# Optimization experiments

Measured on AMD Instinct MI355X. Metric: run time of the kernel, lower is better.

Reference implementation:

```python
import jax, jax.numpy as jnp
import numpy as np

H = 2048   # hidden_size
I = 4096   # intermediate_size (expert_dim_per_shard, world_size=1)
E = 8      # num_local_experts


def setup_inputs() -> dict:
    key = jax.random.key(0)
    ks = jax.random.split(key, 7)
    s = 0.02
    return {
        "hidden_states": jax.random.normal(ks[0], (1, 2048, H), dtype=jnp.float32),
        "router_w": jax.random.normal(ks[1], (H, E), dtype=jnp.float32) * s,
        "gate_up_proj": jax.random.normal(ks[2], (E, H, 2 * I), dtype=jnp.float32) * s,
        "down_proj": jax.random.normal(ks[3], (E, I, H), dtype=jnp.float32) * s,
        "shared_gate_w": jax.random.normal(ks[4], (H, I), dtype=jnp.float32) * s,
        "shared_up_w": jax.random.normal(ks[5], (H, I), dtype=jnp.float32) * s,
        "shared_down_w": jax.random.normal(ks[6], (I, H), dtype=jnp.float32) * s,
        "top_k": 1,
    }


def reference(hidden_states, router_w, gate_up_proj, down_proj,
              shared_gate_w, shared_up_w, shared_down_w, top_k):
    b, s, h = hidden_states.shape
    hs = hidden_states.reshape(-1, h)                      # [T, H]
    T = hs.shape[0]

    # router + topk scatter (non-topk -> -inf so sigmoid -> 0)
    logits = hs @ router_w                                 # [T, E]
    top_v, top_i = jax.lax.top_k(logits, top_k)            # [T, k]
    neg_inf = jnp.full_like(logits, -jnp.inf)
    rows = jnp.arange(T)[:, None]
    router_scores = neg_inf.at[rows, top_i].set(top_v).T   # [E, T]
    router_scores = jax.nn.sigmoid(router_scores.astype(jnp.float32)).astype(hs.dtype)

    # dense dispatch: every token to every expert, scaled by (mostly zero) scores
    routed_in = hs[None, :, :] * router_scores[:, :, None]  # [E, T, H]

    # per-expert grouped GEMM (SwiGLU)
    gate_up = jnp.einsum('eth,ehf->etf', routed_in, gate_up_proj)  # [E, T, 2I]
    gate, up = jnp.split(gate_up, 2, axis=-1)
    routed_out = jnp.einsum('eti,eih->eth', up * jax.nn.silu(gate), down_proj)  # [E, T, H]

    # shared expert (SwiGLU MLP)
    shared = (jax.nn.silu(hs @ shared_gate_w) * (hs @ shared_up_w)) @ shared_down_w  # [T, H]

    # scatter_add over arange indices == sum over experts
    out = shared + routed_out.sum(axis=0)                  # [T, H]
    return out, router_scores
```

## Files before the change

kernel.cpp:

```cpp
#include <hip/hip_runtime.h>
#include <hip/hip_bf16.h>

#define H_DIM 2048
#define E_NUM 8
#define I_DIM 4096
#define TWO_I 8192
#define T_TOK 2048

#define BM 128
#define BN 64
#define BK 64

typedef __bf16 bf16x8 __attribute__((ext_vector_type(8)));
typedef float f32x4 __attribute__((ext_vector_type(4)));

static __device__ __forceinline__ unsigned short f2bs(float x) {
    __hip_bfloat16 h = __float2bfloat16(x);
    return __builtin_bit_cast(unsigned short, h);
}

#define GLL(gsrc, ldst) __builtin_amdgcn_global_load_lds( \
    (const __attribute__((address_space(1))) void*)(gsrc), \
    (__attribute__((address_space(3))) void*)(ldst), 16, 0, 0)

#define MFMA16(a, b, c) __builtin_amdgcn_mfma_f32_16x16x32_bf16(a, b, c, 0, 0, 0)
#define BSWZ(n) (((((n) & 7) ^ (((n) >> 2) & 7))) << 4)
#define A_SRC_CHUNK(lane) ((((lane) & 7) ^ (((lane) >> 3) & 7)) * 8)
#define BARRIER() asm volatile("s_waitcnt lgkmcnt(0)\ns_barrier" ::: "memory")

static __device__ __forceinline__ bf16x8 bload(
    const unsigned short* __restrict__ Bs, int n, int s, int h) {
    int off = (n * 128 + s * 64 + h * 16) ^ BSWZ(n);
    return *reinterpret_cast<const bf16x8*>((const char*)Bs + off);
}

static __device__ __forceinline__ bf16x8 aload(
    const unsigned short* __restrict__ As, int row, int s, int h) {
    int off = row * 128 + ((s * 64 + h * 16) ^ ((row & 7) << 4));
    return *reinterpret_cast<const bf16x8*>((const char*)As + off);
}

__global__ __launch_bounds__(256) void router_convert_kernel(
    const float* __restrict__ hs, const float* __restrict__ rw,
    float* __restrict__ out_scores, int* __restrict__ eidx,
    unsigned short* __restrict__ xb, unsigned short* __restrict__ xs) {
    int tok = blockIdx.x * 4 + (threadIdx.x >> 6);
    int lane = threadIdx.x & 63;
    const float* row = hs + (size_t)tok * H_DIM;
    float4 v[8];
    float acc[E_NUM];
#pragma unroll
    for (int e = 0; e < E_NUM; e++) acc[e] = 0.f;
#pragma unroll
    for (int i = 0; i < 8; i++) {
        int hb = i * 256 + lane * 4;
        v[i] = *reinterpret_cast<const float4*>(row + hb);
        const float* w0 = rw + (size_t)hb * E_NUM;
#pragma unroll
        for (int e = 0; e < E_NUM; e++) {
            acc[e] += v[i].x * w0[e] + v[i].y * w0[E_NUM + e] +
                      v[i].z * w0[2 * E_NUM + e] + v[i].w * w0[3 * E_NUM + e];
        }
    }
#pragma unroll
    for (int e = 0; e < E_NUM; e++) {
#pragma unroll
        for (int o = 32; o > 0; o >>= 1) acc[e] += __shfl_xor(acc[e], o, 64);
    }
    int best = 0; float bv = acc[0];
#pragma unroll
    for (int e = 1; e < E_NUM; e++) { if (acc[e] > bv) { bv = acc[e]; best = e; } }
    float sc = 1.f / (1.f + expf(-bv));
    if (lane < E_NUM) out_scores[(size_t)lane * T_TOK + tok] = (lane == best) ? sc : 0.f;
    if (lane == 0) eidx[tok] = best;
    unsigned short* xbr = xb + (size_t)tok * H_DIM;
    unsigned short* xsr = xs + (size_t)tok * H_DIM;
#pragma unroll
    for (int i = 0; i < 8; i++) {
        int hb = i * 256 + lane * 4;
        ushort4 b, s4;
        b.x = f2bs(v[i].x); b.y = f2bs(v[i].y); b.z = f2bs(v[i].z); b.w = f2bs(v[i].w);
        s4.x = f2bs(v[i].x * sc); s4.y = f2bs(v[i].y * sc);
        s4.z = f2bs(v[i].z * sc); s4.w = f2bs(v[i].w * sc);
        *reinterpret_cast<ushort4*>(xbr + hb) = b;
        *reinterpret_cast<ushort4*>(xsr + hb) = s4;
    }
}

__global__ void group_kernel(const int* __restrict__ eidx, int* __restrict__ perm,
                             int* __restrict__ off) {
    __shared__ int cnt[E_NUM];
    __shared__ int base[E_NUM];
    int t = threadIdx.x;
    if (t < E_NUM) cnt[t] = 0;
    __syncthreads();
    for (int i = t; i < T_TOK; i += 256) atomicAdd(&cnt[eidx[i]], 1);
    __syncthreads();
    if (t == 0) {
        int s = 0;
        for (int e = 0; e < E_NUM; e++) { base[e] = s; off[e] = s; s += cnt[e]; }
        off[E_NUM] = s;
    }
    __syncthreads();
    for (int i = t; i < T_TOK; i += 256) {
        int e = eidx[i];
        int p = atomicAdd(&base[e], 1);
        perm[p] = i;
    }
}

__global__ __launch_bounds__(256, 3) void gemm1_kernel(
    const unsigned short* __restrict__ xb, const unsigned short* __restrict__ xs,
    const float* __restrict__ gup, const float* __restrict__ sg,
    const float* __restrict__ su, const int* __restrict__ perm,
    const int* __restrict__ off, unsigned short* __restrict__ hmid) {
    int nt = blockIdx.x;
    int g = blockIdx.y >> 4;
    int mt = blockIdx.y & 15;
    int rowbase, ng;
    if (g < E_NUM) { rowbase = off[g]; ng = off[g + 1] - rowbase; }
    else { rowbase = 0; ng = T_TOK; }
    int mstart = mt * BM;
    if (mstart >= ng) return;

    __shared__ unsigned short As[2][BM * BK];
    __shared__ unsigned short Bg[BN * BK];
    __shared__ unsigned short Bu[BN * BK];

    int tid = threadIdx.x;
    int wave = tid >> 6, lane = tid & 63;
    int h = lane >> 4, ln = lane & 15;

    const unsigned short* Abase = (g == E_NUM) ? xb : xs;
    unsigned int aoff[4];
#pragma unroll
    for (int j = 0; j < 4; j++) {
        int r = wave * 32 + j * 8 + (lane >> 3);
        int sr = mstart + r; sr = (sr < ng) ? sr : (ng - 1);
        int tokr = (g < E_NUM) ? perm[rowbase + sr] : sr;
        aoff[j] = (unsigned int)tokr * H_DIM + A_SRC_CHUNK(lane);
    }
    int n0 = nt * BN;
    const float* gbase;
    const float* ubase;
    size_t ldb;
    if (g < E_NUM) {
        gbase = gup + (size_t)g * H_DIM * TWO_I + n0;
        ubase = gbase + I_DIM;
        ldb = TWO_I;
    } else {
        gbase = sg + n0;
        ubase = su + n0;
        ldb = I_DIM;
    }
    int k0i = wave * 16 + ((lane >> 4) << 2);
    int nb = (lane & 15) << 2;
    const float* pg = gbase + (size_t)k0i * ldb + nb;
    const float* pu = ubase + (size_t)k0i * ldb + nb;

    f32x4 zero = {0.f, 0.f, 0.f, 0.f};
    f32x4 accg[2][4], accu[2][4];
#pragma unroll
    for (int i = 0; i < 2; i++)
#pragma unroll
        for (int j = 0; j < 4; j++) { accg[i][j] = zero; accu[i][j] = zero; }

    const int NT = H_DIM / BK;
    f32x4 qg0, qg1, qg2, qg3, qu0, qu1, qu2, qu3;

#define G1_QLOAD(t_) { size_t ko_ = (size_t)(t_) * BK * ldb; \
        const float* p_ = pg + ko_; \
        qg0 = *reinterpret_cast<const f32x4*>(p_); \
        qg1 = *reinterpret_cast<const f32x4*>(p_ + ldb); \
        qg2 = *reinterpret_cast<const f32x4*>(p_ + 2 * ldb); \
        qg3 = *reinterpret_cast<const f32x4*>(p_ + 3 * ldb); \
        p_ = pu + ko_; \
        qu0 = *reinterpret_cast<const f32x4*>(p_); \
        qu1 = *reinterpret_cast<const f32x4*>(p_ + ldb); \
        qu2 = *reinterpret_cast<const f32x4*>(p_ + 2 * ldb); \
        qu3 = *reinterpret_cast<const f32x4*>(p_ + 3 * ldb); }
#define G1_BWRITE() { _Pragma("unroll") \
        for (int i_ = 0; i_ < 4; i_++) { int n_ = nb + i_; \
            ushort4 og_, ou_; \
            og_.x = f2bs(qg0[i_]); og_.y = f2bs(qg1[i_]); \
            og_.z = f2bs(qg2[i_]); og_.w = f2bs(qg3[i_]); \
            ou_.x = f2bs(qu0[i_]); ou_.y = f2bs(qu1[i_]); \
            ou_.z = f2bs(qu2[i_]); ou_.w = f2bs(qu3[i_]); \
            int ob_ = (n_ * 128 + k0i * 2) ^ BSWZ(n_); \
            *reinterpret_cast<ushort4*>((char*)Bg + ob_) = og_; \
            *reinterpret_cast<ushort4*>((char*)Bu + ob_) = ou_; } }
#define G1_AGLL(t_, buf_) { _Pragma("unroll") \
        for (int j_ = 0; j_ < 4; j_++) \
            GLL(Abase + aoff[j_] + (unsigned)(t_) * BK, \
                &As[buf_][(wave * 32 + j_ * 8) * BK]); }

    G1_QLOAD(0);
    G1_AGLL(0, 0);
    asm volatile("s_waitcnt vmcnt(0)" ::: "memory");
    G1_BWRITE();
    G1_AGLL(1, 1);
    G1_QLOAD(1);
    BARRIER();

    for (int t = 0; t < NT; ++t) {
        const unsigned short* Ab = &As[t & 1][0];
#pragma unroll
        for (int s = 0; s < 2; s++) {
            bf16x8 a0 = aload(Ab, wave * 32 + 0 * 16 + ln, s, h);
            bf16x8 a1 = aload(Ab, wave * 32 + 1 * 16 + ln, s, h);
#pragma unroll
            for (int j = 0; j < 4; j++) {
                bf16x8 bg = bload(Bg, j * 16 + ln, s, h);
                accg[0][j] = MFMA16(a0, bg, accg[0][j]);
                accg[1][j] = MFMA16(a1, bg, accg[1][j]);
            }
#pragma unroll
            for (int j = 0; j < 4; j++) {
                bf16x8 bu = bload(Bu, j * 16 + ln, s, h);
                accu[0][j] = MFMA16(a0, bu, accu[0][j]);
                accu[1][j] = MFMA16(a1, bu, accu[1][j]);
            }
        }
        BARRIER();
        if (t + 1 < NT) {
            G1_BWRITE();
            int tc = t + 2; if (tc > NT - 1) tc = NT - 1;
            G1_AGLL(tc, t & 1);
            G1_QLOAD(tc);
            BARRIER();
        }
    }

    int hbase = (g < E_NUM) ? rowbase : T_TOK;
#pragma unroll
    for (int i = 0; i < 2; i++) {
#pragma unroll
        for (int j = 0; j < 4; j++) {
#pragma unroll
            for (int r = 0; r < 4; r++) {
                int row = wave * 32 + i * 16 + h * 4 + r;
                int sr = mstart + row;
                if (sr < ng) {
                    float gv = accg[i][j][r], uv = accu[i][j][r];
                    float hv = gv / (1.f + expf(-gv)) * uv;
                    int col = n0 + j * 16 + ln;
                    hmid[(size_t)(hbase + sr) * I_DIM + col] = f2bs(hv);
                }
            }
        }
    }
}

template <int ADD>
__global__ __launch_bounds__(256, 4) void gemm2_kernel(
    const unsigned short* __restrict__ hmid, const float* __restrict__ dwn,
    const float* __restrict__ sd, const int* __restrict__ perm,
    const int* __restrict__ off, float* __restrict__ out) {
    int nt = blockIdx.x;
    int g, mt, rowbase, ng, hbase;
    if (ADD) {
        g = blockIdx.y >> 4; mt = blockIdx.y & 15;
        rowbase = off[g]; ng = off[g + 1] - rowbase; hbase = rowbase;
    } else {
        g = E_NUM; mt = blockIdx.y; rowbase = 0; ng = T_TOK; hbase = T_TOK;
    }
    int mstart = mt * BM;
    if (mstart >= ng) return;

    __shared__ unsigned short As[2][BM * BK];
    __shared__ unsigned short Bs[BN * BK];

    int tid = threadIdx.x;
    int wave = tid >> 6, lane = tid & 63;
    int h = lane >> 4, ln = lane & 15;

    unsigned int aoff[4];
#pragma unroll
    for (int j = 0; j < 4; j++) {
        int r = wave * 32 + j * 8 + (lane >> 3);
        int sr = mstart + r; sr = (sr < ng) ? sr : (ng - 1);
        aoff[j] = (unsigned int)(hbase + sr) * I_DIM + A_SRC_CHUNK(lane);
    }
    int n0 = nt * BN;
    const float* bbase = ADD ? (dwn + (size_t)g * I_DIM * H_DIM + n0) : (sd + n0);
    const size_t ldb = H_DIM;
    int k0i = wave * 16 + ((lane >> 4) << 2);
    int nb = (lane & 15) << 2;
    const float* pb = bbase + (size_t)k0i * ldb + nb;

    f32x4 zero = {0.f, 0.f, 0.f, 0.f};
    f32x4 acc[2][4];
#pragma unroll
    for (int i = 0; i < 2; i++)
#pragma unroll
        for (int j = 0; j < 4; j++) acc[i][j] = zero;

    const int NT2 = I_DIM / BK;
    f32x4 qb0, qb1, qb2, qb3;

#define G2_QLOAD(t_) { size_t ko_ = (size_t)(t_) * BK * ldb; \
        const float* p_ = pb + ko_; \
        qb0 = *reinterpret_cast<const f32x4*>(p_); \
        qb1 = *reinterpret_cast<const f32x4*>(p_ + ldb); \
        qb2 = *reinterpret_cast<const f32x4*>(p_ + 2 * ldb); \
        qb3 = *reinterpret_cast<const f32x4*>(p_ + 3 * ldb); }
#define G2_BWRITE() { _Pragma("unroll") \
        for (int i_ = 0; i_ < 4; i_++) { int n_ = nb + i_; \
            ushort4 o_; \
            o_.x = f2bs(qb0[i_]); o_.y = f2bs(qb1[i_]); \
            o_.z = f2bs(qb2[i_]); o_.w = f2bs(qb3[i_]); \
            int ob_ = (n_ * 128 + k0i * 2) ^ BSWZ(n_); \
            *reinterpret_cast<ushort4*>((char*)Bs + ob_) = o_; } }
#define G2_AGLL(t_, buf_) { _Pragma("unroll") \
        for (int j_ = 0; j_ < 4; j_++) \
            GLL(hmid + aoff[j_] + (unsigned)(t_) * BK, \
                &As[buf_][(wave * 32 + j_ * 8) * BK]); }

    G2_QLOAD(0);
    G2_AGLL(0, 0);
    asm volatile("s_waitcnt vmcnt(0)" ::: "memory");
    G2_BWRITE();
    G2_AGLL(1, 1);
    G2_QLOAD(1);
    BARRIER();

    for (int t = 0; t < NT2; ++t) {
        const unsigned short* Ab = &As[t & 1][0];
#pragma unroll
        for (int s = 0; s < 2; s++) {
            bf16x8 a0 = aload(Ab, wave * 32 + 0 * 16 + ln, s, h);
            bf16x8 a1 = aload(Ab, wave * 32 + 1 * 16 + ln, s, h);
#pragma unroll
            for (int j = 0; j < 4; j++) {
                bf16x8 b = bload(Bs, j * 16 + ln, s, h);
                acc[0][j] = MFMA16(a0, b, acc[0][j]);
                acc[1][j] = MFMA16(a1, b, acc[1][j]);
            }
        }
        BARRIER();
        if (t + 1 < NT2) {
            G2_BWRITE();
            int tc = t + 2; if (tc > NT2 - 1) tc = NT2 - 1;
            G2_AGLL(tc, t & 1);
            G2_QLOAD(tc);
            BARRIER();
        }
    }

#pragma unroll
    for (int i = 0; i < 2; i++) {
#pragma unroll
        for (int j = 0; j < 4; j++) {
#pragma unroll
            for (int r = 0; r < 4; r++) {
                int row = wave * 32 + i * 16 + h * 4 + r;
                int sr = mstart + row;
                if (sr < ng) {
                    int tok = ADD ? perm[rowbase + sr] : sr;
                    int col = n0 + j * 16 + ln;
                    float v = acc[i][j][r];
                    float* o = out + (size_t)tok * H_DIM + col;
                    if (ADD) *o += v; else *o = v;
                }
            }
        }
    }
}

extern "C" void kernel_launch(void* const* d_in, const int* in_sizes, int n_in,
                              void* d_out, int out_size, void* d_ws, size_t ws_size,
                              hipStream_t stream) {
    (void)in_sizes; (void)n_in; (void)out_size;
    const float* hs  = (const float*)d_in[0];
    const float* rw  = (const float*)d_in[1];
    const float* gup = (const float*)d_in[2];
    const float* dwn = (const float*)d_in[3];
    const float* sg  = (const float*)d_in[4];
    const float* su  = (const float*)d_in[5];
    const float* sd  = (const float*)d_in[6];
    float* out = (float*)d_out;
    float* out_scores = out + (size_t)T_TOK * H_DIM;

    char* w = (char*)d_ws;
    size_t o = 0;
    auto alloc = [&](size_t bytes) {
        void* p = w + o;
        o += (bytes + 255) & ~(size_t)255;
        return p;
    };
    unsigned short* xb   = (unsigned short*)alloc((size_t)T_TOK * H_DIM * 2);
    unsigned short* xs   = (unsigned short*)alloc((size_t)T_TOK * H_DIM * 2);
    unsigned short* hmid = (unsigned short*)alloc((size_t)2 * T_TOK * I_DIM * 2);
    int* eidx    = (int*)alloc(T_TOK * 4);
    int* perm    = (int*)alloc(T_TOK * 4);
    int* off     = (int*)alloc(64 * 4);
    if (ws_size < o) return;

    router_convert_kernel<<<T_TOK / 4, 256, 0, stream>>>(hs, rw, out_scores, eidx, xb, xs);
    group_kernel<<<1, 256, 0, stream>>>(eidx, perm, off);

    gemm1_kernel<<<dim3(I_DIM / BN, 9 * 16), 256, 0, stream>>>(
        xb, xs, gup, sg, su, perm, off, hmid);
    gemm2_kernel<0><<<dim3(H_DIM / BN, 16), 256, 0, stream>>>(hmid, dwn, sd, perm, off, out);
    gemm2_kernel<1><<<dim3(H_DIM / BN, E_NUM * 16), 256, 0, stream>>>(hmid, dwn, sd, perm, off, out);
}
```

Measured before the change: 537.6 us.

## Double M tile to 256 rows with 512-thread blocks to halve weight re-reads

Raises BM from 128 to 256 and launches 512-thread blocks (8 waves), halving the number of M tiles per expert and the grid's y dimension. Each fp32 weight tile is then loaded and converted to bf16 once per 256 tokens instead of 128, with each thread loading two k-rows instead of four. This targets the redundant global traffic and conversion cost on the weight matrices. The risk is that partially filled expert tiles waste more work, and the larger blocks with launch_bounds(512,4) could add register pressure or lower occupancy.

```diff
diff --git a/kernel.cpp b/kernel.cpp
--- a/kernel.cpp
+++ b/kernel.cpp
@@ -7,7 +7,7 @@
 #define TWO_I 8192
 #define T_TOK 2048
 
-#define BM 128
+#define BM 256
 #define BN 64
 #define BK 64
 
@@ -109,14 +109,14 @@
     }
 }
 
-__global__ __launch_bounds__(256, 3) void gemm1_kernel(
+__global__ __launch_bounds__(512, 4) void gemm1_kernel(
     const unsigned short* __restrict__ xb, const unsigned short* __restrict__ xs,
     const float* __restrict__ gup, const float* __restrict__ sg,
     const float* __restrict__ su, const int* __restrict__ perm,
     const int* __restrict__ off, unsigned short* __restrict__ hmid) {
     int nt = blockIdx.x;
-    int g = blockIdx.y >> 4;
-    int mt = blockIdx.y & 15;
+    int g = blockIdx.y >> 3;
+    int mt = blockIdx.y & 7;
     int rowbase, ng;
     if (g < E_NUM) { rowbase = off[g]; ng = off[g + 1] - rowbase; }
     else { rowbase = 0; ng = T_TOK; }
@@ -153,8 +153,8 @@
         ubase = su + n0;
         ldb = I_DIM;
     }
-    int k0i = wave * 16 + ((lane >> 4) << 2);
-    int nb = (lane & 15) << 2;
+    int k0i = (tid >> 4) * 2;
+    int nb = (tid & 15) * 4;
     const float* pg = gbase + (size_t)k0i * ldb + nb;
     const float* pu = ubase + (size_t)k0i * ldb + nb;
 
@@ -166,29 +166,20 @@
         for (int j = 0; j < 4; j++) { accg[i][j] = zero; accu[i][j] = zero; }
 
     const int NT = H_DIM / BK;
-    f32x4 qg0, qg1, qg2, qg3, qu0, qu1, qu2, qu3;
+    f32x4 qg0, qg1, qu0, qu1;
 
 #define G1_QLOAD(t_) { size_t ko_ = (size_t)(t_) * BK * ldb; \
-        const float* p_ = pg + ko_; \
-        qg0 = *reinterpret_cast<const f32x4*>(p_); \
-        qg1 = *reinterpret_cast<const f32x4*>(p_ + ldb); \
-        qg2 = *reinterpret_cast<const f32x4*>(p_ + 2 * ldb); \
-        qg3 = *reinterpret_cast<const f32x4*>(p_ + 3 * ldb); \
-        p_ = pu + ko_; \
-        qu0 = *reinterpret_cast<const f32x4*>(p_); \
-        qu1 = *reinterpret_cast<const f32x4*>(p_ + ldb); \
-        qu2 = *reinterpret_cast<const f32x4*>(p_ + 2 * ldb); \
-        qu3 = *reinterpret_cast<const f32x4*>(p_ + 3 * ldb); }
+        qg0 = *reinterpret_cast<const f32x4*>(pg + ko_); \
+        qg1 = *reinterpret_cast<const f32x4*>(pg + ko_ + ldb); \
+        qu0 = *reinterpret_cast<const f32x4*>(pu + ko_); \
+        qu1 = *reinterpret_cast<const f32x4*>(pu + ko_ + ldb); }
 #define G1_BWRITE() { _Pragma("unroll") \
         for (int i_ = 0; i_ < 4; i_++) { int n_ = nb + i_; \
-            ushort4 og_, ou_; \
-            og_.x = f2bs(qg0[i_]); og_.y = f2bs(qg1[i_]); \
-            og_.z = f2bs(qg2[i_]); og_.w = f2bs(qg3[i_]); \
-            ou_.x = f2bs(qu0[i_]); ou_.y = f2bs(qu1[i_]); \
-            ou_.z = f2bs(qu2[i_]); ou_.w = f2bs(qu3[i_]); \
+            unsigned og_ = (unsigned)f2bs(qg0[i_]) | ((unsigned)f2bs(qg1[i_]) << 16); \
+            unsigned ou_ = (unsigned)f2bs(qu0[i_]) | ((unsigned)f2bs(qu1[i_]) << 16); \
             int ob_ = (n_ * 128 + k0i * 2) ^ BSWZ(n_); \
-            *reinterpret_cast<ushort4*>((char*)Bg + ob_) = og_; \
-            *reinterpret_cast<ushort4*>((char*)Bu + ob_) = ou_; } }
+            *reinterpret_cast<unsigned*>((char*)Bg + ob_) = og_; \
+            *reinterpret_cast<unsigned*>((char*)Bu + ob_) = ou_; } }
 #define G1_AGLL(t_, buf_) { _Pragma("unroll") \
         for (int j_ = 0; j_ < 4; j_++) \
             GLL(Abase + aoff[j_] + (unsigned)(t_) * BK, \
@@ -252,14 +243,14 @@
 }
 
 template <int ADD>
-__global__ __launch_bounds__(256, 4) void gemm2_kernel(
+__global__ __launch_bounds__(512, 4) void gemm2_kernel(
     const unsigned short* __restrict__ hmid, const float* __restrict__ dwn,
     const float* __restrict__ sd, const int* __restrict__ perm,
     const int* __restrict__ off, float* __restrict__ out) {
     int nt = blockIdx.x;
     int g, mt, rowbase, ng, hbase;
     if (ADD) {
-        g = blockIdx.y >> 4; mt = blockIdx.y & 15;
+        g = blockIdx.y >> 3; mt = blockIdx.y & 7;
         rowbase = off[g]; ng = off[g + 1] - rowbase; hbase = rowbase;
     } else {
         g = E_NUM; mt = blockIdx.y; rowbase = 0; ng = T_TOK; hbase = T_TOK;
@@ -284,8 +275,8 @@
     int n0 = nt * BN;
     const float* bbase = ADD ? (dwn + (size_t)g * I_DIM * H_DIM + n0) : (sd + n0);
     const size_t ldb = H_DIM;
-    int k0i = wave * 16 + ((lane >> 4) << 2);
-    int nb = (lane & 15) << 2;
+    int k0i = (tid >> 4) * 2;
+    int nb = (tid & 15) * 4;
     const float* pb = bbase + (size_t)k0i * ldb + nb;
 
     f32x4 zero = {0.f, 0.f, 0.f, 0.f};
@@ -296,21 +287,16 @@
         for (int j = 0; j < 4; j++) acc[i][j] = zero;
 
     const int NT2 = I_DIM / BK;
-    f32x4 qb0, qb1, qb2, qb3;
+    f32x4 qb0, qb1;
 
 #define G2_QLOAD(t_) { size_t ko_ = (size_t)(t_) * BK * ldb; \
-        const float* p_ = pb + ko_; \
-        qb0 = *reinterpret_cast<const f32x4*>(p_); \
-        qb1 = *reinterpret_cast<const f32x4*>(p_ + ldb); \
-        qb2 = *reinterpret_cast<const f32x4*>(p_ + 2 * ldb); \
-        qb3 = *reinterpret_cast<const f32x4*>(p_ + 3 * ldb); }
+        qb0 = *reinterpret_cast<const f32x4*>(pb + ko_); \
+        qb1 = *reinterpret_cast<const f32x4*>(pb + ko_ + ldb); }
 #define G2_BWRITE() { _Pragma("unroll") \
         for (int i_ = 0; i_ < 4; i_++) { int n_ = nb + i_; \
-            ushort4 o_; \
-            o_.x = f2bs(qb0[i_]); o_.y = f2bs(qb1[i_]); \
-            o_.z = f2bs(qb2[i_]); o_.w = f2bs(qb3[i_]); \
+            unsigned o_ = (unsigned)f2bs(qb0[i_]) | ((unsigned)f2bs(qb1[i_]) << 16); \
             int ob_ = (n_ * 128 + k0i * 2) ^ BSWZ(n_); \
-            *reinterpret_cast<ushort4*>((char*)Bs + ob_) = o_; } }
+            *reinterpret_cast<unsigned*>((char*)Bs + ob_) = o_; } }
 #define G2_AGLL(t_, buf_) { _Pragma("unroll") \
         for (int j_ = 0; j_ < 4; j_++) \
             GLL(hmid + aoff[j_] + (unsigned)(t_) * BK, \
@@ -399,8 +385,8 @@
     router_convert_kernel<<<T_TOK / 4, 256, 0, stream>>>(hs, rw, out_scores, eidx, xb, xs);
     group_kernel<<<1, 256, 0, stream>>>(eidx, perm, off);
 
-    gemm1_kernel<<<dim3(I_DIM / BN, 9 * 16), 256, 0, stream>>>(
+    gemm1_kernel<<<dim3(I_DIM / BN, 9 * 8), 512, 0, stream>>>(
         xb, xs, gup, sg, su, perm, off, hmid);
-    gemm2_kernel<0><<<dim3(H_DIM / BN, 16), 256, 0, stream>>>(hmid, dwn, sd, perm, off, out);
-    gemm2_kernel<1><<<dim3(H_DIM / BN, E_NUM * 16), 256, 0, stream>>>(hmid, dwn, sd, perm, off, out);
-}
+    gemm2_kernel<0><<<dim3(H_DIM / BN, 8), 512, 0, stream>>>(hmid, dwn, sd, perm, off, out);
+    gemm2_kernel<1><<<dim3(H_DIM / BN, E_NUM * 8), 512, 0, stream>>>(hmid, dwn, sd, perm, off, out);
+}
```

Measured after the change: 488.7 us. 1.1x faster.
